# Kernel optimization log

Hardware: AMD Instinct MI355X
Metric: run time of the kernel (lower is better)

## Reference

```python
import jax, jax.numpy as jnp
import numpy as np

N_NODES = 100000
N_EDGES = 1600000
D = 128  # node_feat_size == edge_hidden_size


def setup_inputs() -> dict:
    key = jax.random.key(0)
    ks = jax.random.split(key, 10)
    s = 1.0 / np.sqrt(D)
    return {
        "node_feats": jax.random.normal(ks[0], (N_NODES, D), jnp.float32),
        "edge_logits": jax.random.normal(ks[1], (N_EDGES, 1), jnp.float32),
        "W_proj": jax.random.normal(ks[2], (D, D), jnp.float32) * s,
        "b_proj": jax.random.normal(ks[3], (D,), jnp.float32) * s,
        "W1": jax.random.normal(ks[4], (2 * D, D), jnp.float32) * s,
        "b1": jax.random.normal(ks[5], (D,), jnp.float32) * s,
        "W2": jax.random.normal(ks[6], (D, D), jnp.float32) * s,
        "b2": jax.random.normal(ks[7], (D,), jnp.float32) * s,
        "src": jax.random.randint(ks[8], (N_EDGES,), 0, N_NODES),
        "dst": jax.random.randint(ks[9], (N_EDGES,), 0, N_NODES),
    }


def reference(node_feats, edge_logits, W_proj, b_proj, W1, b1, W2, b2, src, dst):
    # ---- edge_softmax: softmax of edge_logits grouped by destination node ----
    # [E,1] logits; per-dst max for numerical stability (gradient-free shift)
    m = jax.ops.segment_max(edge_logits, dst, num_segments=N_NODES)  # [N,1]
    m = jnp.where(jnp.isfinite(m), m, 0.0)  # nodes with no in-edges
    e = jnp.exp(edge_logits - jax.lax.stop_gradient(m)[dst])  # [E,1]
    z = jax.ops.segment_sum(e, dst, num_segments=N_NODES)  # [N,1]
    a = e / z[dst]  # [E,1]

    # ---- project_node (dropout is identity at inference) ----
    hv = node_feats @ W_proj + b_proj  # [N,D]

    # ---- src_mul_edge + sum aggregation: c[v] = sum_{(u->v)} a_uv * hv[u] ----
    msg = hv[src] * a  # [E,D]
    c = jax.ops.segment_sum(msg, dst, num_segments=N_NODES)  # [N,D]

    context = jax.nn.elu(c)
    x = jnp.concatenate([context, node_feats], axis=1)  # [N,2D]
    h = jax.nn.relu(x @ W1 + b1)  # Linear -> Dropout(id) -> ReLU
    out = jax.nn.relu(h @ W2 + b2)  # Linear -> Dropout(id), outer ReLU
    return out
```

## Files before the change

kernel.cpp:

```cpp
#include <hip/hip_runtime.h>
#include <hip/hip_bf16.h>

typedef __hip_bfloat16 bf16;
typedef __attribute__((ext_vector_type(8))) __bf16 bf16x8;
typedef __attribute__((ext_vector_type(4))) float floatx4;

#define BUCKET_SHIFT 7
#define BUCKET_NODES 128
#define MAX_NB 1024
#define CAST_BLOCKS 512

__device__ __forceinline__ unsigned short f2b(float f) {
    bf16 h = __float2bfloat16(f);
    unsigned short s;
    __builtin_memcpy(&s, &h, 2);
    return s;
}
__device__ __forceinline__ float b2f(unsigned short u) {
    unsigned int x = ((unsigned int)u) << 16;
    float f;
    __builtin_memcpy(&f, &x, 4);
    return f;
}
__device__ __forceinline__ float load_dual(const void* p, long long i, bool isbf) {
    return isbf ? b2f(((const unsigned short*)p)[i]) : ((const float*)p)[i];
}
__device__ __forceinline__ bf16x8 ldsfrag(const unsigned short* p) {
    union { uint4 u; bf16x8 v; } t;
    t.u = *(const uint4*)p;
    return t.v;
}
__device__ __forceinline__ bf16x8 gfrag_dual(const void* A, int row, int stride, int k0, bool isbf) {
    if (isbf) {
        union { uint4 u; bf16x8 v; } t;
        t.u = *(const uint4*)((const unsigned short*)A + (size_t)row * stride + k0);
        return t.v;
    }
    const float* ap = (const float*)A + (size_t)row * stride + k0;
    float4 v0 = ((const float4*)ap)[0];
    float4 v1 = ((const float4*)ap)[1];
    union { unsigned short s[8]; bf16x8 v; } t;
    t.s[0] = f2b(v0.x); t.s[1] = f2b(v0.y); t.s[2] = f2b(v0.z); t.s[3] = f2b(v0.w);
    t.s[4] = f2b(v1.x); t.s[5] = f2b(v1.y); t.s[6] = f2b(v1.z); t.s[7] = f2b(v1.w);
    return t.v;
}

__global__ __launch_bounds__(64) void detect_kernel(const unsigned int* __restrict__ words,
                                                    int* __restrict__ flag,
                                                    int* __restrict__ bcount) {
    for (int i = threadIdx.x; i < MAX_NB; i += 64) bcount[i] = 0;
    int cnt = 0;
    for (int i = threadIdx.x; i < 4096; i += 64) {
        unsigned int lo = words[i] & 0xFFFFu;
        unsigned int e = (lo >> 7) & 0xFFu;
        if (lo == 0u || (e >= 110u && e <= 135u)) cnt++;
    }
#pragma unroll
    for (int off = 32; off > 0; off >>= 1) cnt += __shfl_down(cnt, off, 64);
    if (threadIdx.x == 0) *flag = (cnt > 2458) ? 1 : 0;
}

__global__ __launch_bounds__(256) void transpose_all_kernel(const void* __restrict__ Wp,
                                                            const void* __restrict__ W1,
                                                            const void* __restrict__ W2,
                                                            unsigned short* __restrict__ Wtp,
                                                            unsigned short* __restrict__ Wt1,
                                                            unsigned short* __restrict__ Wt2,
                                                            const int* __restrict__ flag) {
    bool isbf = (*flag != 0);
    int idx = blockIdx.x * 256 + threadIdx.x;
    if (idx < 16384) {
        int n = idx >> 7, k = idx & 127;
        Wtp[idx] = f2b(load_dual(Wp, (long long)k * 128 + n, isbf));
    } else if (idx < 49152) {
        int j = idx - 16384;
        int n = j >> 8, k = j & 255;
        Wt1[j] = f2b(load_dual(W1, (long long)k * 128 + n, isbf));
    } else if (idx < 65536) {
        int j = idx - 49152;
        int n = j >> 7, k = j & 127;
        Wt2[j] = f2b(load_dual(W2, (long long)k * 128 + n, isbf));
    }
}

__global__ __launch_bounds__(256) void cast_hist_kernel(const void* __restrict__ nf,
                                                        unsigned short* __restrict__ nfb,
                                                        const int* __restrict__ dst,
                                                        int* __restrict__ bcount,
                                                        const int* __restrict__ flag,
                                                        int E, int N) {
    const bool isbf = (*flag != 0);
    if (blockIdx.x < CAST_BLOCKS) {
        const int units = N * 16;
        for (int u = blockIdx.x * 256 + threadIdx.x; u < units; u += CAST_BLOCKS * 256) {
            if (isbf) {
                ((uint4*)nfb)[u] = ((const uint4*)nf)[u];
            } else {
                const float* ap = (const float*)nf + (size_t)u * 8;
                float4 v0 = ((const float4*)ap)[0];
                float4 v1 = ((const float4*)ap)[1];
                union { uint4 q; unsigned short s[8]; } P;
                P.s[0] = f2b(v0.x); P.s[1] = f2b(v0.y); P.s[2] = f2b(v0.z); P.s[3] = f2b(v0.w);
                P.s[4] = f2b(v1.x); P.s[5] = f2b(v1.y); P.s[6] = f2b(v1.z); P.s[7] = f2b(v1.w);
                ((uint4*)nfb)[u] = P.q;
            }
        }
        return;
    }
    __shared__ int lcnt[MAX_NB];
    for (int i = threadIdx.x; i < MAX_NB; i += 256) lcnt[i] = 0;
    __syncthreads();
    int base = (blockIdx.x - CAST_BLOCKS) * 8192;
#pragma unroll
    for (int j = 0; j < 32; ++j) {
        int e = base + j * 256 + threadIdx.x;
        if (e < E) atomicAdd(&lcnt[dst[e] >> BUCKET_SHIFT], 1);
    }
    __syncthreads();
    for (int i = threadIdx.x; i < MAX_NB; i += 256)
        if (lcnt[i]) atomicAdd(&bcount[i], lcnt[i]);
}

__global__ __launch_bounds__(256) void bscan_kernel(const int* __restrict__ bcount,
                                                    int* __restrict__ bstart,
                                                    int* __restrict__ bcursor, int NB) {
    int t = threadIdx.x;
    int v[4];
    int sum = 0;
#pragma unroll
    for (int j = 0; j < 4; ++j) {
        int i = t * 4 + j;
        v[j] = (i < NB) ? bcount[i] : 0;
        sum += v[j];
    }
    int lane = t & 63, wave = t >> 6;
    int inc = sum;
#pragma unroll
    for (int off = 1; off < 64; off <<= 1) {
        int x = __shfl_up(inc, off, 64);
        if (lane >= off) inc += x;
    }
    __shared__ int wsum[4];
    if (lane == 63) wsum[wave] = inc;
    __syncthreads();
    int woff = 0;
    for (int w = 0; w < wave; ++w) woff += wsum[w];
    int run = inc - sum + woff;
#pragma unroll
    for (int j = 0; j < 4; ++j) {
        int i = t * 4 + j;
        if (i < NB) { bstart[i] = run; bcursor[i] = run; }
        run += v[j];
    }
}

__global__ __launch_bounds__(256) void bappend_kernel(const int* __restrict__ dst,
                                                      const int* __restrict__ src,
                                                      const void* __restrict__ logits,
                                                      int* __restrict__ bcursor,
                                                      uint2* __restrict__ ebuf,
                                                      const int* __restrict__ flag, int E) {
    __shared__ int lcnt[MAX_NB];
    __shared__ int lbase[MAX_NB];
    for (int i = threadIdx.x; i < MAX_NB; i += 256) lcnt[i] = 0;
    __syncthreads();
    const bool isbf = (*flag != 0);
    int base = blockIdx.x * 8192;
#pragma unroll
    for (int j = 0; j < 32; ++j) {
        int e = base + j * 256 + threadIdx.x;
        if (e < E) atomicAdd(&lcnt[dst[e] >> BUCKET_SHIFT], 1);
    }
    __syncthreads();
    for (int i = threadIdx.x; i < MAX_NB; i += 256) {
        int c = lcnt[i];
        if (c) { lbase[i] = atomicAdd(&bcursor[i], c); lcnt[i] = 0; }
    }
    __syncthreads();
#pragma unroll
    for (int j = 0; j < 32; ++j) {
        int e = base + j * 256 + threadIdx.x;
        if (e < E) {
            int d = dst[e];
            int b = d >> BUCKET_SHIFT;
            float w = expf(load_dual(logits, e, isbf));
            int pos = lbase[b] + atomicAdd(&lcnt[b], 1);
            uint2 rec;
            rec.x = (unsigned int)src[e] | ((unsigned int)(d & (BUCKET_NODES - 1)) << 24);
            rec.y = __float_as_uint(w);
            ebuf[pos] = rec;
        }
    }
}

__global__ __launch_bounds__(256) void bcsr_kernel(const uint2* __restrict__ ebuf,
                                                   const int* __restrict__ bstart,
                                                   const int* __restrict__ bcount,
                                                   uint2* __restrict__ ebuf2,
                                                   int* __restrict__ row_start,
                                                   int* __restrict__ ncount, int N) {
    __shared__ int lcnt[BUCKET_NODES];
    __shared__ int lbase[BUCKET_NODES];
    const int b = blockIdx.x;
    const int s0 = bstart[b];
    const int cnt = bcount[b];
    if (threadIdx.x < BUCKET_NODES) lcnt[threadIdx.x] = 0;
    __syncthreads();
    for (int i = threadIdx.x; i < cnt; i += 256)
        atomicAdd(&lcnt[ebuf[s0 + i].x >> 24], 1);
    __syncthreads();
    if (threadIdx.x < 64) {
        int lane = threadIdx.x;
        int carry = 0;
#pragma unroll
        for (int half = 0; half < 2; ++half) {
            int idx = half * 64 + lane;
            int v = lcnt[idx];
            int inc = v;
#pragma unroll
            for (int off = 1; off < 64; off <<= 1) {
                int t = __shfl_up(inc, off, 64);
                if (lane >= off) inc += t;
            }
            lbase[idx] = carry + inc - v;
            carry += __shfl(inc, 63, 64);
        }
    }
    __syncthreads();
    if (threadIdx.x < BUCKET_NODES) {
        int gn = b * BUCKET_NODES + threadIdx.x;
        if (gn < N) {
            row_start[gn] = s0 + lbase[threadIdx.x];
            ncount[gn] = lcnt[threadIdx.x];
        }
    }
    __syncthreads();
    if (threadIdx.x < BUCKET_NODES) lcnt[threadIdx.x] = 0;
    __syncthreads();
    for (int i = threadIdx.x; i < cnt; i += 256) {
        uint2 rec = ebuf[s0 + i];
        int dl = rec.x >> 24;
        int pos = lbase[dl] + atomicAdd(&lcnt[dl], 1);
        ebuf2[s0 + pos] = make_uint2(rec.x & 0xFFFFFFu, rec.y);
    }
}

__global__ __launch_bounds__(256) void agg_csr_kernel(const int* __restrict__ row_start,
                                                      const int* __restrict__ ncount,
                                                      const uint2* __restrict__ erec,
                                                      const unsigned int* __restrict__ nfb32,
                                                      unsigned int* __restrict__ g32, int N) {
    int n = blockIdx.x * 4 + (threadIdx.x >> 6);
    int lane = threadIdx.x & 63;
    if (n >= N) return;
    int s0 = row_start[n];
    int deg = ncount[n];
    float accx = 0.f, accy = 0.f, z = 0.f;
    int i = 0;
    for (; i + 8 <= deg; i += 8) {
        uint2 r[8];
        unsigned int h[8];
#pragma unroll
        for (int j = 0; j < 8; ++j) r[j] = erec[s0 + i + j];
#pragma unroll
        for (int j = 0; j < 8; ++j) h[j] = nfb32[(size_t)r[j].x * 64 + lane];
#pragma unroll
        for (int j = 0; j < 8; ++j) {
            float w = __uint_as_float(r[j].y);
            z += w;
            accx += w * b2f((unsigned short)h[j]);
            accy += w * b2f((unsigned short)(h[j] >> 16));
        }
    }
    for (; i + 4 <= deg; i += 4) {
        uint2 r[4];
        unsigned int h[4];
#pragma unroll
        for (int j = 0; j < 4; ++j) r[j] = erec[s0 + i + j];
#pragma unroll
        for (int j = 0; j < 4; ++j) h[j] = nfb32[(size_t)r[j].x * 64 + lane];
#pragma unroll
        for (int j = 0; j < 4; ++j) {
            float w = __uint_as_float(r[j].y);
            z += w;
            accx += w * b2f((unsigned short)h[j]);
            accy += w * b2f((unsigned short)(h[j] >> 16));
        }
    }
    for (; i < deg; ++i) {
        uint2 r = erec[s0 + i];
        unsigned int h = nfb32[(size_t)r.x * 64 + lane];
        float w = __uint_as_float(r.y);
        z += w;
        accx += w * b2f((unsigned short)h);
        accy += w * b2f((unsigned short)(h >> 16));
    }
    float rz = (z > 0.f) ? 1.f / z : 0.f;
    g32[(size_t)n * 64 + lane] =
        ((unsigned int)f2b(accy * rz) << 16) | f2b(accx * rz);
}

__global__ __launch_bounds__(256) void mega_mlp(const unsigned short* __restrict__ g,
                                                const void* __restrict__ nf,
                                                const int* __restrict__ ncount,
                                                const unsigned short* __restrict__ Wtp,
                                                const void* __restrict__ bp,
                                                const unsigned short* __restrict__ Wt1,
                                                const void* __restrict__ b1,
                                                const unsigned short* __restrict__ Wt2,
                                                const void* __restrict__ b2,
                                                void* __restrict__ outp,
                                                const int* __restrict__ flag, int N) {
    __shared__ unsigned short Wl[128 * 72];
    __shared__ unsigned short Hl[4][32 * 136];
    const bool isbf = (*flag != 0);
    const int t = threadIdx.x, wid = t >> 6, lane = t & 63;
    const int m16 = lane & 15, quad = lane >> 4;
    const int row0 = blockIdx.x * 128;

    floatx4 acc[2][8];
#pragma unroll
    for (int i = 0; i < 2; ++i)
#pragma unroll
        for (int j = 0; j < 8; ++j) acc[i][j] = (floatx4){0.f, 0.f, 0.f, 0.f};

    int ra0 = row0 + wid * 32 + m16;      if (ra0 >= N) ra0 = N - 1;
    int ra1 = row0 + wid * 32 + 16 + m16; if (ra1 >= N) ra1 = N - 1;

#pragma unroll
    for (int kc = 0; kc < 2; ++kc) {
        {
            int r = t >> 1, kh = (t & 1) * 32;
            const uint4* s = (const uint4*)(Wtp + (size_t)r * 128 + kc * 64 + kh);
            uint4* d = (uint4*)&Wl[r * 72 + kh];
#pragma unroll
            for (int q = 0; q < 4; ++q) d[q] = s[q];
        }
        __syncthreads();
#pragma unroll
        for (int c = 0; c < 2; ++c) {
            int kl = c * 32 + quad * 8;
            int ka = kc * 64 + kl;
            union { uint4 u; bf16x8 v; } t0, t1;
            t0.u = *(const uint4*)(g + (size_t)ra0 * 128 + ka);
            t1.u = *(const uint4*)(g + (size_t)ra1 * 128 + ka);
#pragma unroll
            for (int nt = 0; nt < 8; ++nt) {
                bf16x8 b = ldsfrag(&Wl[(nt * 16 + m16) * 72 + kl]);
                acc[0][nt] = __builtin_amdgcn_mfma_f32_16x16x32_bf16(t0.v, b, acc[0][nt], 0, 0, 0);
                acc[1][nt] = __builtin_amdgcn_mfma_f32_16x16x32_bf16(t1.v, b, acc[1][nt], 0, 0, 0);
            }
        }
        __syncthreads();
    }

#pragma unroll
    for (int mt = 0; mt < 2; ++mt) {
#pragma unroll
        for (int rg = 0; rg < 4; ++rg) {
            int lr = mt * 16 + quad * 4 + rg;
            int gr = row0 + wid * 32 + lr;
            if (gr >= N) gr = N - 1;
            int deg = ncount[gr];
#pragma unroll
            for (int nt = 0; nt < 8; ++nt) {
                int col = nt * 16 + m16;
                float x = 0.f;
                if (deg > 0) {
                    x = acc[mt][nt][rg] + load_dual(bp, col, isbf);
                    x = x > 0.f ? x : expm1f(x);
                }
                Hl[wid][lr * 136 + col] = f2b(x);
            }
        }
    }

#pragma unroll
    for (int i = 0; i < 2; ++i)
#pragma unroll
        for (int j = 0; j < 8; ++j) acc[i][j] = (floatx4){0.f, 0.f, 0.f, 0.f};

#pragma unroll
    for (int kc = 0; kc < 4; ++kc) {
        {
            int r = t >> 1, kh = (t & 1) * 32;
            const uint4* s = (const uint4*)(Wt1 + (size_t)r * 256 + kc * 64 + kh);
            uint4* d = (uint4*)&Wl[r * 72 + kh];
#pragma unroll
            for (int q = 0; q < 4; ++q) d[q] = s[q];
        }
        __syncthreads();
#pragma unroll
        for (int c = 0; c < 2; ++c) {
            int kl = c * 32 + quad * 8;
            int ka = kc * 64 + kl;
            bf16x8 a0, a1;
            if (ka < 128) {
                a0 = ldsfrag(&Hl[wid][m16 * 136 + ka]);
                a1 = ldsfrag(&Hl[wid][(16 + m16) * 136 + ka]);
            } else {
                a0 = gfrag_dual(nf, ra0, 128, ka - 128, isbf);
                a1 = gfrag_dual(nf, ra1, 128, ka - 128, isbf);
            }
#pragma unroll
            for (int nt = 0; nt < 8; ++nt) {
                bf16x8 b = ldsfrag(&Wl[(nt * 16 + m16) * 72 + kl]);
                acc[0][nt] = __builtin_amdgcn_mfma_f32_16x16x32_bf16(a0, b, acc[0][nt], 0, 0, 0);
                acc[1][nt] = __builtin_amdgcn_mfma_f32_16x16x32_bf16(a1, b, acc[1][nt], 0, 0, 0);
            }
        }
        __syncthreads();
    }

#pragma unroll
    for (int nt = 0; nt < 8; ++nt) {
        int col = nt * 16 + m16;
        float bb = load_dual(b1, col, isbf);
#pragma unroll
        for (int mt = 0; mt < 2; ++mt) {
#pragma unroll
            for (int rg = 0; rg < 4; ++rg) {
                int lr = mt * 16 + quad * 4 + rg;
                float x = acc[mt][nt][rg] + bb;
                Hl[wid][lr * 136 + col] = f2b(x > 0.f ? x : 0.f);
            }
        }
    }

#pragma unroll
    for (int i = 0; i < 2; ++i)
#pragma unroll
        for (int j = 0; j < 8; ++j) acc[i][j] = (floatx4){0.f, 0.f, 0.f, 0.f};

#pragma unroll
    for (int kc = 0; kc < 2; ++kc) {
        {
            int r = t >> 1, kh = (t & 1) * 32;
            const uint4* s = (const uint4*)(Wt2 + (size_t)r * 128 + kc * 64 + kh);
            uint4* d = (uint4*)&Wl[r * 72 + kh];
#pragma unroll
            for (int q = 0; q < 4; ++q) d[q] = s[q];
        }
        __syncthreads();
#pragma unroll
        for (int c = 0; c < 2; ++c) {
            int kl = c * 32 + quad * 8;
            int ka = kc * 64 + kl;
            bf16x8 a0 = ldsfrag(&Hl[wid][m16 * 136 + ka]);
            bf16x8 a1 = ldsfrag(&Hl[wid][(16 + m16) * 136 + ka]);
#pragma unroll
            for (int nt = 0; nt < 8; ++nt) {
                bf16x8 b = ldsfrag(&Wl[(nt * 16 + m16) * 72 + kl]);
                acc[0][nt] = __builtin_amdgcn_mfma_f32_16x16x32_bf16(a0, b, acc[0][nt], 0, 0, 0);
                acc[1][nt] = __builtin_amdgcn_mfma_f32_16x16x32_bf16(a1, b, acc[1][nt], 0, 0, 0);
            }
        }
        __syncthreads();
    }

#pragma unroll
    for (int mt = 0; mt < 2; ++mt) {
        int gr0 = row0 + wid * 32 + mt * 16 + quad * 4;
#pragma unroll
        for (int nt = 0; nt < 8; ++nt) {
            int col = nt * 16 + m16;
            float bb = load_dual(b2, col, isbf);
#pragma unroll
            for (int rg = 0; rg < 4; ++rg) {
                int gr = gr0 + rg;
                if (gr < N) {
                    float x = acc[mt][nt][rg] + bb;
                    x = x > 0.f ? x : 0.f;
                    if (!isbf) ((float*)outp)[(size_t)gr * 128 + col] = x;
                    else       ((unsigned short*)outp)[(size_t)gr * 128 + col] = f2b(x);
                }
            }
        }
    }
}

extern "C" void kernel_launch(void* const* d_in, const int* in_sizes, int n_in,
                              void* d_out, int out_size, void* d_ws, size_t ws_size,
                              hipStream_t stream) {
    const void* node_feats  = d_in[0];
    const void* edge_logits = d_in[1];
    const void* W_proj      = d_in[2];
    const void* b_proj      = d_in[3];
    const void* W1          = d_in[4];
    const void* b1          = d_in[5];
    const void* W2          = d_in[6];
    const void* b2          = d_in[7];
    const int*  src         = (const int*)d_in[8];
    const int*  dst         = (const int*)d_in[9];

    const int N = in_sizes[0] / 128;
    const int E = in_sizes[8];
    const int NB = (N + BUCKET_NODES - 1) / BUCKET_NODES;

    char* ws = (char*)d_ws;
    size_t off = 0;
    unsigned short* nfb = (unsigned short*)(ws + off); off += (size_t)N * 256;
    unsigned short* g   = (unsigned short*)(ws + off); off += (size_t)N * 256;
    uint2* ebuf  = (uint2*)(ws + off); off += (size_t)E * 8;
    uint2* ebuf2 = (uint2*)(ws + off); off += (size_t)E * 8;
    unsigned short* Wtp = (unsigned short*)(ws + off); off += 128 * 128 * 2;
    unsigned short* Wt1 = (unsigned short*)(ws + off); off += 128 * 256 * 2;
    unsigned short* Wt2 = (unsigned short*)(ws + off); off += 128 * 128 * 2;
    int* bcount    = (int*)(ws + off); off += MAX_NB * 4;
    int* bstart    = (int*)(ws + off); off += MAX_NB * 4;
    int* bcursor   = (int*)(ws + off); off += MAX_NB * 4;
    int* row_start = (int*)(ws + off); off += (size_t)N * 4;
    int* ncount    = (int*)(ws + off); off += (size_t)N * 4;
    int* flag      = (int*)(ws + off);

    const int gblocks = (N + 127) / 128;
    const int ebblocks = (E + 8191) / 8192;

    detect_kernel<<<1, 64, 0, stream>>>((const unsigned int*)node_feats, flag, bcount);
    transpose_all_kernel<<<256, 256, 0, stream>>>(W_proj, W1, W2, Wtp, Wt1, Wt2, flag);

    cast_hist_kernel<<<CAST_BLOCKS + ebblocks, 256, 0, stream>>>(
        node_feats, nfb, dst, bcount, flag, E, N);
    bscan_kernel<<<1, 256, 0, stream>>>(bcount, bstart, bcursor, NB);
    bappend_kernel<<<ebblocks, 256, 0, stream>>>(dst, src, edge_logits, bcursor,
                                                 ebuf, flag, E);
    bcsr_kernel<<<NB, 256, 0, stream>>>(ebuf, bstart, bcount, ebuf2,
                                        row_start, ncount, N);

    agg_csr_kernel<<<(N + 3) / 4, 256, 0, stream>>>(row_start, ncount, ebuf2,
                                                    (const unsigned int*)nfb,
                                                    (unsigned int*)g, N);

    mega_mlp<<<gblocks, 256, 0, stream>>>(g, node_feats, ncount, Wtp, b_proj,
                                          Wt1, b1, Wt2, b2, d_out, flag, N);
}
```

Before: 354.7 us.

## Fuse prep kernels, use per-block histograms, and sort+aggregate buckets in LDS

Merges dtype detection, weight transpose, feature cast and dst histogram into one prep kernel, with each block detecting the dtype flag locally. Per-block partial histograms replace global atomics and are reduced in the scan kernel. The separate bucket-CSR pass and the CSR aggregation kernel become one kernel that counting-sorts each 128-node bucket's edges inside LDS and aggregates directly, so the second edge buffer and its global round trip go away. The cost is an O(cnt) scan per node in the fallback path when a bucket overflows LDS capacity, and lower occupancy from the large LDS footprint and 512-thread blocks.

New measurement: 364.4 us. 1.03x slower.

```diff
diff --git a/kernel.cpp b/kernel.cpp
--- a/kernel.cpp
+++ b/kernel.cpp
@@ -9,6 +9,8 @@
 #define BUCKET_NODES 128
 #define MAX_NB 1024
 #define CAST_BLOCKS 512
+#define TRANS_BLOCKS 64
+#define CAP 2816
 
 __device__ __forceinline__ unsigned short f2b(float f) {
     bf16 h = __float2bfloat16(f);
@@ -45,54 +47,62 @@
     return t.v;
 }
 
-__global__ __launch_bounds__(64) void detect_kernel(const unsigned int* __restrict__ words,
-                                                    int* __restrict__ flag,
-                                                    int* __restrict__ bcount) {
-    for (int i = threadIdx.x; i < MAX_NB; i += 64) bcount[i] = 0;
-    int cnt = 0;
-    for (int i = threadIdx.x; i < 4096; i += 64) {
-        unsigned int lo = words[i] & 0xFFFFu;
-        unsigned int e = (lo >> 7) & 0xFFu;
-        if (lo == 0u || (e >= 110u && e <= 135u)) cnt++;
-    }
-#pragma unroll
-    for (int off = 32; off > 0; off >>= 1) cnt += __shfl_down(cnt, off, 64);
-    if (threadIdx.x == 0) *flag = (cnt > 2458) ? 1 : 0;
-}
-
-__global__ __launch_bounds__(256) void transpose_all_kernel(const void* __restrict__ Wp,
-                                                            const void* __restrict__ W1,
-                                                            const void* __restrict__ W2,
-                                                            unsigned short* __restrict__ Wtp,
-                                                            unsigned short* __restrict__ Wt1,
-                                                            unsigned short* __restrict__ Wt2,
-                                                            const int* __restrict__ flag) {
-    bool isbf = (*flag != 0);
-    int idx = blockIdx.x * 256 + threadIdx.x;
-    if (idx < 16384) {
-        int n = idx >> 7, k = idx & 127;
-        Wtp[idx] = f2b(load_dual(Wp, (long long)k * 128 + n, isbf));
-    } else if (idx < 49152) {
-        int j = idx - 16384;
-        int n = j >> 8, k = j & 255;
-        Wt1[j] = f2b(load_dual(W1, (long long)k * 128 + n, isbf));
-    } else if (idx < 65536) {
-        int j = idx - 49152;
-        int n = j >> 7, k = j & 127;
-        Wt2[j] = f2b(load_dual(W2, (long long)k * 128 + n, isbf));
-    }
-}
-
-__global__ __launch_bounds__(256) void cast_hist_kernel(const void* __restrict__ nf,
-                                                        unsigned short* __restrict__ nfb,
-                                                        const int* __restrict__ dst,
-                                                        int* __restrict__ bcount,
-                                                        const int* __restrict__ flag,
-                                                        int E, int N) {
-    const bool isbf = (*flag != 0);
-    if (blockIdx.x < CAST_BLOCKS) {
+__device__ __forceinline__ bool block_flag(const unsigned int* words, int* sflag) {
+    if (threadIdx.x < 64) {
+        int cnt = 0;
+        for (int i = threadIdx.x; i < 1024; i += 64) {
+            unsigned int lo = words[i] & 0xFFFFu;
+            unsigned int e = (lo >> 7) & 0xFFu;
+            if (lo == 0u || (e >= 110u && e <= 135u)) cnt++;
+        }
+#pragma unroll
+        for (int off = 32; off > 0; off >>= 1) cnt += __shfl_down(cnt, off, 64);
+        if (threadIdx.x == 0) *sflag = (cnt > 614) ? 1 : 0;
+    }
+    __syncthreads();
+    return *sflag != 0;
+}
+
+__global__ __launch_bounds__(256) void prep_kernel(const void* __restrict__ nf,
+                                                   const void* __restrict__ Wp,
+                                                   const void* __restrict__ W1,
+                                                   const void* __restrict__ W2,
+                                                   const int* __restrict__ dst,
+                                                   unsigned short* __restrict__ nfb,
+                                                   unsigned short* __restrict__ Wtp,
+                                                   unsigned short* __restrict__ Wt1,
+                                                   unsigned short* __restrict__ Wt2,
+                                                   int* __restrict__ hpart,
+                                                   int* __restrict__ flagp,
+                                                   int E, int N) {
+    __shared__ int lcnt[MAX_NB];
+    __shared__ int sflag;
+    const bool isbf = block_flag((const unsigned int*)nf, &sflag);
+
+    if (blockIdx.x < TRANS_BLOCKS) {
+        if (blockIdx.x == 0 && threadIdx.x == 0) *flagp = isbf ? 1 : 0;
+#pragma unroll
+        for (int j = 0; j < 4; ++j) {
+            int idx = blockIdx.x * 1024 + j * 256 + threadIdx.x;
+            if (idx < 16384) {
+                int n = idx >> 7, k = idx & 127;
+                Wtp[idx] = f2b(load_dual(Wp, (long long)k * 128 + n, isbf));
+            } else if (idx < 49152) {
+                int jj = idx - 16384;
+                int n = jj >> 8, k = jj & 255;
+                Wt1[jj] = f2b(load_dual(W1, (long long)k * 128 + n, isbf));
+            } else {
+                int jj = idx - 49152;
+                int n = jj >> 7, k = jj & 127;
+                Wt2[jj] = f2b(load_dual(W2, (long long)k * 128 + n, isbf));
+            }
+        }
+        return;
+    }
+    if (blockIdx.x < TRANS_BLOCKS + CAST_BLOCKS) {
+        const int cb = blockIdx.x - TRANS_BLOCKS;
         const int units = N * 16;
-        for (int u = blockIdx.x * 256 + threadIdx.x; u < units; u += CAST_BLOCKS * 256) {
+        for (int u = cb * 256 + threadIdx.x; u < units; u += CAST_BLOCKS * 256) {
             if (isbf) {
                 ((uint4*)nfb)[u] = ((const uint4*)nf)[u];
             } else {
@@ -107,10 +117,10 @@
         }
         return;
     }
-    __shared__ int lcnt[MAX_NB];
+    const int p = blockIdx.x - TRANS_BLOCKS - CAST_BLOCKS;
     for (int i = threadIdx.x; i < MAX_NB; i += 256) lcnt[i] = 0;
     __syncthreads();
-    int base = (blockIdx.x - CAST_BLOCKS) * 8192;
+    int base = p * 8192;
 #pragma unroll
     for (int j = 0; j < 32; ++j) {
         int e = base + j * 256 + threadIdx.x;
@@ -118,21 +128,21 @@
     }
     __syncthreads();
     for (int i = threadIdx.x; i < MAX_NB; i += 256)
-        if (lcnt[i]) atomicAdd(&bcount[i], lcnt[i]);
-}
-
-__global__ __launch_bounds__(256) void bscan_kernel(const int* __restrict__ bcount,
+        hpart[p * MAX_NB + i] = lcnt[i];
+}
+
+__global__ __launch_bounds__(256) void bscan_kernel(const int* __restrict__ hpart,
                                                     int* __restrict__ bstart,
-                                                    int* __restrict__ bcursor, int NB) {
+                                                    int* __restrict__ bcursor, int HB) {
     int t = threadIdx.x;
-    int v[4];
-    int sum = 0;
-#pragma unroll
-    for (int j = 0; j < 4; ++j) {
-        int i = t * 4 + j;
-        v[j] = (i < NB) ? bcount[i] : 0;
-        sum += v[j];
-    }
+    const uint4* hp4 = (const uint4*)hpart;
+    uint4 a = make_uint4(0, 0, 0, 0);
+    for (int p = 0; p < HB; ++p) {
+        uint4 h = hp4[p * 256 + t];
+        a.x += h.x; a.y += h.y; a.z += h.z; a.w += h.w;
+    }
+    int v[4] = {(int)a.x, (int)a.y, (int)a.z, (int)a.w};
+    int sum = v[0] + v[1] + v[2] + v[3];
     int lane = t & 63, wave = t >> 6;
     int inc = sum;
 #pragma unroll
@@ -149,9 +159,11 @@
 #pragma unroll
     for (int j = 0; j < 4; ++j) {
         int i = t * 4 + j;
-        if (i < NB) { bstart[i] = run; bcursor[i] = run; }
+        bstart[i] = run;
+        bcursor[i] = run;
         run += v[j];
     }
+    if (t == 255) bstart[MAX_NB] = run;
 }
 
 __global__ __launch_bounds__(256) void bappend_kernel(const int* __restrict__ dst,
@@ -193,111 +205,126 @@
     }
 }
 
-__global__ __launch_bounds__(256) void bcsr_kernel(const uint2* __restrict__ ebuf,
-                                                   const int* __restrict__ bstart,
-                                                   const int* __restrict__ bcount,
-                                                   uint2* __restrict__ ebuf2,
-                                                   int* __restrict__ row_start,
-                                                   int* __restrict__ ncount, int N) {
+__global__ __launch_bounds__(512) void sort_agg_kernel(const uint2* __restrict__ ebuf,
+                                                       const int* __restrict__ bstart,
+                                                       const unsigned int* __restrict__ nfb32,
+                                                       unsigned int* __restrict__ g32,
+                                                       int* __restrict__ ncount, int N) {
+    __shared__ unsigned int recx[CAP];
+    __shared__ float recw[CAP];
+    __shared__ unsigned short sidx[CAP];
     __shared__ int lcnt[BUCKET_NODES];
-    __shared__ int lbase[BUCKET_NODES];
+    __shared__ int lbase[BUCKET_NODES + 1];
     const int b = blockIdx.x;
     const int s0 = bstart[b];
-    const int cnt = bcount[b];
-    if (threadIdx.x < BUCKET_NODES) lcnt[threadIdx.x] = 0;
-    __syncthreads();
-    for (int i = threadIdx.x; i < cnt; i += 256)
-        atomicAdd(&lcnt[ebuf[s0 + i].x >> 24], 1);
-    __syncthreads();
-    if (threadIdx.x < 64) {
-        int lane = threadIdx.x;
-        int carry = 0;
-#pragma unroll
-        for (int half = 0; half < 2; ++half) {
-            int idx = half * 64 + lane;
-            int v = lcnt[idx];
-            int inc = v;
-#pragma unroll
-            for (int off = 1; off < 64; off <<= 1) {
-                int t = __shfl_up(inc, off, 64);
-                if (lane >= off) inc += t;
-            }
-            lbase[idx] = carry + inc - v;
-            carry += __shfl(inc, 63, 64);
-        }
-    }
-    __syncthreads();
-    if (threadIdx.x < BUCKET_NODES) {
-        int gn = b * BUCKET_NODES + threadIdx.x;
-        if (gn < N) {
-            row_start[gn] = s0 + lbase[threadIdx.x];
-            ncount[gn] = lcnt[threadIdx.x];
-        }
-    }
-    __syncthreads();
-    if (threadIdx.x < BUCKET_NODES) lcnt[threadIdx.x] = 0;
-    __syncthreads();
-    for (int i = threadIdx.x; i < cnt; i += 256) {
-        uint2 rec = ebuf[s0 + i];
-        int dl = rec.x >> 24;
-        int pos = lbase[dl] + atomicAdd(&lcnt[dl], 1);
-        ebuf2[s0 + pos] = make_uint2(rec.x & 0xFFFFFFu, rec.y);
-    }
-}
-
-__global__ __launch_bounds__(256) void agg_csr_kernel(const int* __restrict__ row_start,
-                                                      const int* __restrict__ ncount,
-                                                      const uint2* __restrict__ erec,
-                                                      const unsigned int* __restrict__ nfb32,
-                                                      unsigned int* __restrict__ g32, int N) {
-    int n = blockIdx.x * 4 + (threadIdx.x >> 6);
-    int lane = threadIdx.x & 63;
-    if (n >= N) return;
-    int s0 = row_start[n];
-    int deg = ncount[n];
-    float accx = 0.f, accy = 0.f, z = 0.f;
-    int i = 0;
-    for (; i + 8 <= deg; i += 8) {
-        uint2 r[8];
-        unsigned int h[8];
-#pragma unroll
-        for (int j = 0; j < 8; ++j) r[j] = erec[s0 + i + j];
-#pragma unroll
-        for (int j = 0; j < 8; ++j) h[j] = nfb32[(size_t)r[j].x * 64 + lane];
-#pragma unroll
-        for (int j = 0; j < 8; ++j) {
-            float w = __uint_as_float(r[j].y);
-            z += w;
-            accx += w * b2f((unsigned short)h[j]);
-            accy += w * b2f((unsigned short)(h[j] >> 16));
-        }
-    }
-    for (; i + 4 <= deg; i += 4) {
-        uint2 r[4];
-        unsigned int h[4];
-#pragma unroll
-        for (int j = 0; j < 4; ++j) r[j] = erec[s0 + i + j];
-#pragma unroll
-        for (int j = 0; j < 4; ++j) h[j] = nfb32[(size_t)r[j].x * 64 + lane];
-#pragma unroll
-        for (int j = 0; j < 4; ++j) {
-            float w = __uint_as_float(r[j].y);
-            z += w;
-            accx += w * b2f((unsigned short)h[j]);
-            accy += w * b2f((unsigned short)(h[j] >> 16));
-        }
-    }
-    for (; i < deg; ++i) {
-        uint2 r = erec[s0 + i];
-        unsigned int h = nfb32[(size_t)r.x * 64 + lane];
-        float w = __uint_as_float(r.y);
-        z += w;
-        accx += w * b2f((unsigned short)h);
-        accy += w * b2f((unsigned short)(h >> 16));
-    }
-    float rz = (z > 0.f) ? 1.f / z : 0.f;
-    g32[(size_t)n * 64 + lane] =
-        ((unsigned int)f2b(accy * rz) << 16) | f2b(accx * rz);
+    const int cnt = bstart[b + 1] - s0;
+    const int tid = threadIdx.x;
+    const int wid = tid >> 6, lane = tid & 63;
+
+    if (tid < BUCKET_NODES) lcnt[tid] = 0;
+    __syncthreads();
+
+    if (cnt <= CAP) {
+        for (int i = tid; i < cnt; i += 512) {
+            uint2 r = ebuf[s0 + i];
+            recx[i] = r.x;
+            recw[i] = __uint_as_float(r.y);
+            atomicAdd(&lcnt[r.x >> 24], 1);
+        }
+        __syncthreads();
+        if (tid < 64) {
+            int carry = 0;
+#pragma unroll
+            for (int half = 0; half < 2; ++half) {
+                int idx = half * 64 + tid;
+                int v = lcnt[idx];
+                int inc = v;
+#pragma unroll
+                for (int off = 1; off < 64; off <<= 1) {
+                    int t = __shfl_up(inc, off, 64);
+                    if (tid >= off) inc += t;
+                }
+                lbase[idx] = carry + inc - v;
+                carry += __shfl(inc, 63, 64);
+            }
+            if (tid == 0) lbase[BUCKET_NODES] = carry;
+        }
+        __syncthreads();
+        if (tid < BUCKET_NODES) {
+            int gn = b * BUCKET_NODES + tid;
+            if (gn < N) ncount[gn] = lcnt[tid];
+            lcnt[tid] = 0;
+        }
+        __syncthreads();
+        for (int i = tid; i < cnt; i += 512) {
+            int dl = recx[i] >> 24;
+            int pos = lbase[dl] + atomicAdd(&lcnt[dl], 1);
+            sidx[pos] = (unsigned short)i;
+        }
+        __syncthreads();
+        for (int n0 = wid * 16; n0 < wid * 16 + 16; ++n0) {
+            int gn = b * BUCKET_NODES + n0;
+            if (gn >= N) break;
+            int base = lbase[n0];
+            int deg = lbase[n0 + 1] - base;
+            float ax = 0.f, ay = 0.f, z = 0.f;
+            int i = 0;
+            for (; i + 8 <= deg; i += 8) {
+                int ii[8]; unsigned int rx[8]; float w[8]; unsigned int h[8];
+#pragma unroll
+                for (int j = 0; j < 8; ++j) ii[j] = sidx[base + i + j];
+#pragma unroll
+                for (int j = 0; j < 8; ++j) { rx[j] = recx[ii[j]]; w[j] = recw[ii[j]]; }
+#pragma unroll
+                for (int j = 0; j < 8; ++j)
+                    h[j] = nfb32[(size_t)(rx[j] & 0xFFFFFFu) * 64 + lane];
+#pragma unroll
+                for (int j = 0; j < 8; ++j) {
+                    z += w[j];
+                    ax += w[j] * b2f((unsigned short)h[j]);
+                    ay += w[j] * b2f((unsigned short)(h[j] >> 16));
+                }
+            }
+            for (; i < deg; ++i) {
+                int ii = sidx[base + i];
+                unsigned int rx = recx[ii];
+                float w = recw[ii];
+                unsigned int h = nfb32[(size_t)(rx & 0xFFFFFFu) * 64 + lane];
+                z += w;
+                ax += w * b2f((unsigned short)h);
+                ay += w * b2f((unsigned short)(h >> 16));
+            }
+            float rz = (z > 0.f) ? 1.f / z : 0.f;
+            g32[(size_t)gn * 64 + lane] =
+                ((unsigned int)f2b(ay * rz) << 16) | f2b(ax * rz);
+        }
+    } else {
+        for (int i = tid; i < cnt; i += 512)
+            atomicAdd(&lcnt[ebuf[s0 + i].x >> 24], 1);
+        __syncthreads();
+        if (tid < BUCKET_NODES) {
+            int gn = b * BUCKET_NODES + tid;
+            if (gn < N) ncount[gn] = lcnt[tid];
+        }
+        for (int n0 = wid * 16; n0 < wid * 16 + 16; ++n0) {
+            int gn = b * BUCKET_NODES + n0;
+            if (gn >= N) break;
+            float ax = 0.f, ay = 0.f, z = 0.f;
+            for (int i = 0; i < cnt; ++i) {
+                uint2 r = ebuf[s0 + i];
+                if ((int)(r.x >> 24) == n0) {
+                    float w = __uint_as_float(r.y);
+                    unsigned int h = nfb32[(size_t)(r.x & 0xFFFFFFu) * 64 + lane];
+                    z += w;
+                    ax += w * b2f((unsigned short)h);
+                    ay += w * b2f((unsigned short)(h >> 16));
+                }
+            }
+            float rz = (z > 0.f) ? 1.f / z : 0.f;
+            g32[(size_t)gn * 64 + lane] =
+                ((unsigned int)f2b(ay * rz) << 16) | f2b(ax * rz);
+        }
+    }
 }
 
 __global__ __launch_bounds__(256) void mega_mlp(const unsigned short* __restrict__ g,
@@ -496,41 +523,32 @@
     const int N = in_sizes[0] / 128;
     const int E = in_sizes[8];
     const int NB = (N + BUCKET_NODES - 1) / BUCKET_NODES;
+    const int HB = (E + 8191) / 8192;
 
     char* ws = (char*)d_ws;
     size_t off = 0;
     unsigned short* nfb = (unsigned short*)(ws + off); off += (size_t)N * 256;
     unsigned short* g   = (unsigned short*)(ws + off); off += (size_t)N * 256;
-    uint2* ebuf  = (uint2*)(ws + off); off += (size_t)E * 8;
-    uint2* ebuf2 = (uint2*)(ws + off); off += (size_t)E * 8;
+    uint2* ebuf = (uint2*)(ws + off); off += (size_t)E * 8;
     unsigned short* Wtp = (unsigned short*)(ws + off); off += 128 * 128 * 2;
     unsigned short* Wt1 = (unsigned short*)(ws + off); off += 128 * 256 * 2;
     unsigned short* Wt2 = (unsigned short*)(ws + off); off += 128 * 128 * 2;
-    int* bcount    = (int*)(ws + off); off += MAX_NB * 4;
-    int* bstart    = (int*)(ws + off); off += MAX_NB * 4;
-    int* bcursor   = (int*)(ws + off); off += MAX_NB * 4;
-    int* row_start = (int*)(ws + off); off += (size_t)N * 4;
-    int* ncount    = (int*)(ws + off); off += (size_t)N * 4;
-    int* flag      = (int*)(ws + off);
+    int* hpart   = (int*)(ws + off); off += (size_t)HB * MAX_NB * 4;
+    int* bstart  = (int*)(ws + off); off += (MAX_NB + 4) * 4;
+    int* bcursor = (int*)(ws + off); off += MAX_NB * 4;
+    int* ncount  = (int*)(ws + off); off += (size_t)N * 4;
+    int* flag    = (int*)(ws + off);
 
     const int gblocks = (N + 127) / 128;
-    const int ebblocks = (E + 8191) / 8192;
-
-    detect_kernel<<<1, 64, 0, stream>>>((const unsigned int*)node_feats, flag, bcount);
-    transpose_all_kernel<<<256, 256, 0, stream>>>(W_proj, W1, W2, Wtp, Wt1, Wt2, flag);
-
-    cast_hist_kernel<<<CAST_BLOCKS + ebblocks, 256, 0, stream>>>(
-        node_feats, nfb, dst, bcount, flag, E, N);
-    bscan_kernel<<<1, 256, 0, stream>>>(bcount, bstart, bcursor, NB);
-    bappend_kernel<<<ebblocks, 256, 0, stream>>>(dst, src, edge_logits, bcursor,
-                                                 ebuf, flag, E);
-    bcsr_kernel<<<NB, 256, 0, stream>>>(ebuf, bstart, bcount, ebuf2,
-                                        row_start, ncount, N);
-
-    agg_csr_kernel<<<(N + 3) / 4, 256, 0, stream>>>(row_start, ncount, ebuf2,
-                                                    (const unsigned int*)nfb,
-                                                    (unsigned int*)g, N);
-
+
+    prep_kernel<<<TRANS_BLOCKS + CAST_BLOCKS + HB, 256, 0, stream>>>(
+        node_feats, W_proj, W1, W2, dst, nfb, Wtp, Wt1, Wt2, hpart, flag, E, N);
+    bscan_kernel<<<1, 256, 0, stream>>>(hpart, bstart, bcursor, HB);
+    bappend_kernel<<<HB, 256, 0, stream>>>(dst, src, edge_logits, bcursor,
+                                           ebuf, flag, E);
+    sort_agg_kernel<<<NB, 512, 0, stream>>>(ebuf, bstart,
+                                            (const unsigned int*)nfb,
+                                            (unsigned int*)g, ncount, N);
     mega_mlp<<<gblocks, 256, 0, stream>>>(g, node_feats, ncount, Wtp, b_proj,
                                           Wt1, b1, Wt2, b2, d_out, flag, N);
 }
```
